# Performance work log

Hardware: AMD Instinct MI355X
Metric: run time of the kernel (lower is better)

## Reference

```python
import jax, jax.numpy as jnp
import numpy as np

N = 16384      # number of nodes (= in_num_dim)
F_DIM = 512    # node feature dim (= in_node_dim)
EMBED = 128    # embed_dim (D1)
OUT = 64       # out_dim (final latent)
E = 524288     # number of edges (avg degree 32)
GAT_SLOPE = 0.5    # GATConv negative_slope
LRELU_SLOPE = 0.01 # F.leaky_relu default on embed


def setup_inputs() -> dict:
    key = jax.random.key(0)
    ks = jax.random.split(key, 10)
    x = jax.random.normal(ks[0], (N, F_DIM), dtype=jnp.float32)
    edge_index = jax.random.randint(ks[1], (2, E), 0, N, dtype=jnp.int64)
    adj = jnp.zeros((1,), dtype=jnp.float32)  # unused by forward (as in source)
    # GATConv params (single head)
    W_gat = jax.random.normal(ks[2], (F_DIM, OUT), dtype=jnp.float32) / np.sqrt(F_DIM)
    att_src = jax.random.normal(ks[3], (OUT,), dtype=jnp.float32) * 0.1
    att_dst = jax.random.normal(ks[4], (OUT,), dtype=jnp.float32) * 0.1
    b_gat = jnp.zeros((OUT,), dtype=jnp.float32)
    # AttributeAE params: dense1 (N -> EMBED), dense2 (EMBED -> OUT)
    W1 = jax.random.normal(ks[5], (N, EMBED), dtype=jnp.float32) / np.sqrt(N)
    b1 = jnp.zeros((EMBED,), dtype=jnp.float32)
    W2 = jax.random.normal(ks[6], (EMBED, OUT), dtype=jnp.float32) / np.sqrt(EMBED)
    b2 = jnp.zeros((OUT,), dtype=jnp.float32)
    return dict(x=x, edge_index=edge_index, adj=adj, W_gat=W_gat,
                att_src=att_src, att_dst=att_dst, b_gat=b_gat,
                W1=W1, b1=b1, W2=W2, b2=b2)


def _gat_conv(x, edge_index, W_gat, att_src, att_dst, b_gat):
    # PyG GATConv, heads=1, with self-loops appended.
    n = x.shape[0]
    loops = jnp.arange(n, dtype=edge_index.dtype)
    src = jnp.concatenate([edge_index[0], loops])  # message sources j
    dst = jnp.concatenate([edge_index[1], loops])  # aggregation targets i
    h = x @ W_gat                                  # [N, OUT]
    a_src = h @ att_src                            # [N]
    a_dst = h @ att_dst                            # [N]
    e = jax.nn.leaky_relu(a_src[src] + a_dst[dst], GAT_SLOPE)  # [E+N]
    # segment softmax over incoming edges of each dst node
    m = jax.ops.segment_max(e, dst, num_segments=n)
    p = jnp.exp(e - m[dst])
    denom = jax.ops.segment_sum(p, dst, num_segments=n)
    alpha = p / denom[dst]
    out = jax.ops.segment_sum(alpha[:, None] * h[src], dst, num_segments=n)
    return out + b_gat


def _forward(x, edge_index, W_gat, att_src, att_dst, b_gat, W1, b1, W2, b2):
    # StructureAE
    embed_x = jax.nn.leaky_relu(
        _gat_conv(x, edge_index, W_gat, att_src, att_dst, b_gat), LRELU_SLOPE)
    A_hat = jax.nn.sigmoid(embed_x @ embed_x.T)          # [N, N]
    # AttributeAE (dropout = 0 -> identity)
    h1 = jax.nn.relu(x.T @ W1 + b1)                      # [F, EMBED]
    h2 = h1 @ W2 + b2                                    # [F, OUT]
    X_hat = embed_x @ h2.T                               # [N, F]
    return A_hat, X_hat


def reference(x, edge_index, adj, W_gat, att_src, att_dst, b_gat, W1, b1, W2, b2):
    # adj is accepted but unused, matching the torch forward signature
    return _forward(x, edge_index, W_gat, att_src, att_dst, b_gat, W1, b1, W2, b2)
```

## Files before the change

kernel.cpp:

```cpp
#include <hip/hip_runtime.h>
#include <hip/hip_bf16.h>

#define NN 16384
#define FD 512
#define EMB 128
#define OD 64
#define NE 524288

typedef __bf16 bf16x8 __attribute__((ext_vector_type(8)));
typedef float f32x4 __attribute__((ext_vector_type(4)));
typedef unsigned short u16;

__device__ inline float bfu2f(u16 u) {
    unsigned int x = (unsigned int)u << 16;
    float f;
    __builtin_memcpy(&f, &x, 4);
    return f;
}

__global__ __launch_bounds__(256) void k_prep(
    const float* __restrict__ x, __hip_bfloat16* __restrict__ xbf,
    const float* __restrict__ Wg, __hip_bfloat16* __restrict__ WgT,
    const int* __restrict__ ei, int* __restrict__ deg,
    const float* __restrict__ W1, float* __restrict__ part) {
    __shared__ float xs[4][64];
    __shared__ float wsh[4][EMB];
    int b = blockIdx.x;
    int t = threadIdx.x;
    if (b < 256) {
        int fb = b & 7, nc = b >> 3;
        int f0 = fb * 64, nb = nc * 512;
        int eb = (t & 15) * 8;
        int fbase = (t >> 4) * 4;
        float acc[4][8] = {};
        for (int n4 = 0; n4 < 512; n4 += 4) {
            { int nn = t >> 6, ff = t & 63;
              xs[nn][ff] = x[(size_t)(nb + n4 + nn) * FD + f0 + ff]; }
#pragma unroll
            for (int j = 0; j < 2; ++j) {
                int idx = t + j * 256;
                wsh[idx >> 7][idx & 127] = W1[(size_t)(nb + n4 + (idx >> 7)) * EMB + (idx & 127)];
            }
            __syncthreads();
#pragma unroll
            for (int nn = 0; nn < 4; ++nn) {
                float xv[4], wv[8];
#pragma unroll
                for (int i = 0; i < 4; ++i) xv[i] = xs[nn][fbase + i];
#pragma unroll
                for (int j = 0; j < 8; ++j) wv[j] = wsh[nn][eb + j];
#pragma unroll
                for (int i = 0; i < 4; ++i)
#pragma unroll
                    for (int j = 0; j < 8; ++j) acc[i][j] += xv[i] * wv[j];
            }
            __syncthreads();
        }
#pragma unroll
        for (int i = 0; i < 4; ++i) {
            float* dst = &part[((size_t)nc * FD + f0 + fbase + i) * EMB + eb];
            *reinterpret_cast<f32x4*>(dst) = *reinterpret_cast<f32x4*>(&acc[i][0]);
            *reinterpret_cast<f32x4*>(dst + 4) = *reinterpret_cast<f32x4*>(&acc[i][4]);
        }
        return;
    }
    b -= 256;
    if (b < NE / 256) {
        int i = b * 256 + t;
        atomicAdd(deg + ei[NE + i], 1);
        return;
    }
    b -= NE / 256;
    if (b < NN * FD / 2048) {
        size_t i = ((size_t)b * 256 + t) * 8;
        float4 v0 = *reinterpret_cast<const float4*>(x + i);
        float4 v1 = *reinterpret_cast<const float4*>(x + i + 4);
        __hip_bfloat16 o[8];
        o[0] = __float2bfloat16(v0.x); o[1] = __float2bfloat16(v0.y);
        o[2] = __float2bfloat16(v0.z); o[3] = __float2bfloat16(v0.w);
        o[4] = __float2bfloat16(v1.x); o[5] = __float2bfloat16(v1.y);
        o[6] = __float2bfloat16(v1.z); o[7] = __float2bfloat16(v1.w);
        *reinterpret_cast<uint4*>(xbf + i) = *reinterpret_cast<const uint4*>(o);
        return;
    }
    b -= NN * FD / 2048;
    {
        int c = t >> 2;
        int k0 = (t & 3) * 128;
        for (int j = 0; j < 128; ++j)
            WgT[c * 512 + k0 + j] = __float2bfloat16(Wg[(size_t)(k0 + j) * OD + c]);
    }
}

__global__ __launch_bounds__(256) void k_scan(const int* __restrict__ deg,
                                              int* __restrict__ row_start) {
    __shared__ int part[256];
    int t = threadIdx.x;
    int base = t * 64;
    int s = 0;
    for (int j = 0; j < 64; ++j) s += deg[base + j];
    part[t] = s;
    __syncthreads();
    for (int off = 1; off < 256; off <<= 1) {
        int v = (t >= off) ? part[t - off] : 0;
        __syncthreads();
        part[t] += v;
        __syncthreads();
    }
    int run = part[t] - s;
    if (t == 255) row_start[NN] = part[255];
    for (int j = 0; j < 64; ++j) { row_start[base + j] = run; run += deg[base + j]; }
}

__global__ __launch_bounds__(256) void k_mid(
    const int* __restrict__ ei, const int* __restrict__ row_start,
    int* __restrict__ cursor, int* __restrict__ ssrc,
    const __hip_bfloat16* __restrict__ xbf, const __hip_bfloat16* __restrict__ WgT,
    const float* __restrict__ att_s, const float* __restrict__ att_d,
    __hip_bfloat16* __restrict__ hbf, float* __restrict__ a_src, float* __restrict__ a_dst,
    const float* __restrict__ part, const float* __restrict__ b1,
    const float* __restrict__ W2, const float* __restrict__ b2,
    __hip_bfloat16* __restrict__ h2bf) {
    __shared__ float hv[4][EMB];
    int b = blockIdx.x;
    int t = threadIdx.x;
    if (b < NE / 256) {
        int i = b * 256 + t;
        int d = ei[NE + i];
        int pos = atomicAdd(cursor + d, 1);
        ssrc[row_start[d] + pos] = ei[i];
        return;
    }
    b -= NE / 256;
    int w = t >> 6, l = t & 63;
    if (b < NN / 64) {
        int lg = l >> 4, lm = l & 15;
        int r0 = b * 64 + w * 16;
        const bf16x8* Xp = reinterpret_cast<const bf16x8*>(xbf);
        const bf16x8* Wp = reinterpret_cast<const bf16x8*>(WgT);
        bf16x8 a[16];
        size_t abase = (size_t)(r0 + lm) * 64 + lg;
#pragma unroll
        for (int kc = 0; kc < 16; ++kc) a[kc] = Xp[abase + kc * 4];
        f32x4 acc[4];
#pragma unroll
        for (int j = 0; j < 4; ++j) {
            f32x4 c = {0.f, 0.f, 0.f, 0.f};
            size_t bbase = (size_t)(j * 16 + lm) * 64 + lg;
#pragma unroll
            for (int kc = 0; kc < 16; ++kc)
                c = __builtin_amdgcn_mfma_f32_16x16x32_bf16(a[kc], Wp[bbase + kc * 4], c, 0, 0, 0);
            acc[j] = c;
        }
#pragma unroll
        for (int j = 0; j < 4; ++j)
#pragma unroll
            for (int reg = 0; reg < 4; ++reg)
                hbf[(size_t)(r0 + lg * 4 + reg) * OD + j * 16 + lm] = __float2bfloat16(acc[j][reg]);
        float ats0 = att_s[lm], ats1 = att_s[16 + lm], ats2 = att_s[32 + lm], ats3 = att_s[48 + lm];
        float atd0 = att_d[lm], atd1 = att_d[16 + lm], atd2 = att_d[32 + lm], atd3 = att_d[48 + lm];
#pragma unroll
        for (int reg = 0; reg < 4; ++reg) {
            float ps = acc[0][reg] * ats0 + acc[1][reg] * ats1 + acc[2][reg] * ats2 + acc[3][reg] * ats3;
            float pd = acc[0][reg] * atd0 + acc[1][reg] * atd1 + acc[2][reg] * atd2 + acc[3][reg] * atd3;
#pragma unroll
            for (int off = 1; off < 16; off <<= 1) {
                ps += __shfl_xor(ps, off, 64);
                pd += __shfl_xor(pd, off, 64);
            }
            if (lm == 0) {
                int r = r0 + lg * 4 + reg;
                a_src[r] = ps;
                a_dst[r] = pd;
            }
        }
        return;
    }
    b -= NN / 64;
    {
        int f = b * 4 + w;
        float s0 = 0.f, s1 = 0.f;
        for (int nc = 0; nc < 32; ++nc) {
            const float* p = part + ((size_t)nc * FD + f) * EMB;
            s0 += p[l];
            s1 += p[l + 64];
        }
        s0 += b1[l]; s1 += b1[l + 64];
        hv[w][l] = s0 > 0.f ? s0 : 0.f;
        hv[w][l + 64] = s1 > 0.f ? s1 : 0.f;
        __syncthreads();
        float acc = b2[l];
        const float* myhv = hv[w];
        for (int e = 0; e < EMB; ++e)
            acc += myhv[e] * W2[e * OD + l];
        h2bf[(size_t)f * OD + l] = __float2bfloat16(acc);
    }
}

__global__ __launch_bounds__(256) void k_aggcsr(
    const int* __restrict__ row_start, const int* __restrict__ ssrc,
    const float* __restrict__ a_src, const float* __restrict__ a_dst,
    const u16* __restrict__ hb, const float* __restrict__ bg,
    __hip_bfloat16* __restrict__ ebf) {
    int node = blockIdx.x * 4 + (threadIdx.x >> 6);
    int lane = threadIdx.x & 63;
    float ad = a_dst[node];
    float e0 = a_src[node] + ad;
    e0 = e0 > 0.f ? e0 : 0.5f * e0;
    float p0 = __expf(e0);
    float denom = p0;
    float acc = p0 * bfu2f(hb[(size_t)node * OD + lane]);
    int j0 = row_start[node], j1 = row_start[node + 1];
    int j = j0;
    for (; j + 2 <= j1; j += 2) {
        int sA = ssrc[j], sB = ssrc[j + 1];
        float hA = bfu2f(hb[(size_t)sA * OD + lane]);
        float hB = bfu2f(hb[(size_t)sB * OD + lane]);
        float eA = a_src[sA] + ad, eB = a_src[sB] + ad;
        eA = eA > 0.f ? eA : 0.5f * eA;
        eB = eB > 0.f ? eB : 0.5f * eB;
        float pA = __expf(eA), pB = __expf(eB);
        denom += pA + pB;
        acc += pA * hA + pB * hB;
    }
    if (j < j1) {
        int s = ssrc[j];
        float e = a_src[s] + ad;
        e = e > 0.f ? e : 0.5f * e;
        float pv = __expf(e);
        denom += pv;
        acc += pv * bfu2f(hb[(size_t)s * OD + lane]);
    }
    float v = acc * __builtin_amdgcn_rcpf(denom) + bg[lane];
    v = v > 0.f ? v : 0.01f * v;
    ebf[(size_t)node * OD + lane] = __float2bfloat16(v);
}

__global__ __launch_bounds__(256) void k_mmX(const __hip_bfloat16* __restrict__ A,
                                             const __hip_bfloat16* __restrict__ B,
                                             float* __restrict__ out) {
    __shared__ float ls[4][32 * 68];
    int w = threadIdx.x >> 6, l = threadIdx.x & 63;
    int lg = l >> 4, lm = l & 15;
    int i0 = blockIdx.y * 128 + w * 32;
    int j0 = blockIdx.x * 128;
    const bf16x8* Ap = reinterpret_cast<const bf16x8*>(A);
    const bf16x8* Bp = reinterpret_cast<const bf16x8*>(B);
    size_t arow = (size_t)(i0 + lm) * 8;
    bf16x8 a0 = Ap[arow + lg];
    bf16x8 a1 = Ap[arow + 4 + lg];
    bf16x8 a2 = Ap[arow + 128 + lg];
    bf16x8 a3 = Ap[arow + 128 + 4 + lg];
    f32x4 accL[8], accH[8];
#pragma unroll
    for (int ct = 0; ct < 8; ++ct) {
        size_t brow = (size_t)(j0 + ct * 16 + lm) * 8;
        bf16x8 b0 = Bp[brow + lg];
        bf16x8 b1 = Bp[brow + 4 + lg];
        f32x4 cL = {0.f, 0.f, 0.f, 0.f};
        f32x4 cH = {0.f, 0.f, 0.f, 0.f};
        cL = __builtin_amdgcn_mfma_f32_16x16x32_bf16(a0, b0, cL, 0, 0, 0);
        cL = __builtin_amdgcn_mfma_f32_16x16x32_bf16(a1, b1, cL, 0, 0, 0);
        cH = __builtin_amdgcn_mfma_f32_16x16x32_bf16(a2, b0, cH, 0, 0, 0);
        cH = __builtin_amdgcn_mfma_f32_16x16x32_bf16(a3, b1, cH, 0, 0, 0);
        accL[ct] = cL;
        accH[ct] = cH;
    }
    float* myl = ls[w];
#pragma unroll
    for (int ph = 0; ph < 2; ++ph) {
        if (ph == 1) {
            asm volatile("s_waitcnt lgkmcnt(0)" ::: "memory");
            __builtin_amdgcn_sched_barrier(0);
        }
#pragma unroll
        for (int c4 = 0; c4 < 4; ++c4) {
            int ct = ph * 4 + c4;
            int col = c4 * 16 + lm;
#pragma unroll
            for (int reg = 0; reg < 4; ++reg) {
                int row = lg * 4 + reg;
                myl[row * 68 + col] = accL[ct][reg];
                myl[(row + 16) * 68 + col] = accH[ct][reg];
            }
        }
        asm volatile("s_waitcnt lgkmcnt(0)" ::: "memory");
        __builtin_amdgcn_sched_barrier(0);
#pragma unroll
        for (int i = 0; i < 8; ++i) {
            int row = i * 4 + lg;
            f32x4 v = *reinterpret_cast<const f32x4*>(&myl[row * 68 + lm * 4]);
            float* dst = &out[(size_t)(i0 + row) * FD + j0 + ph * 64 + lm * 4];
            __builtin_nontemporal_store(v, reinterpret_cast<f32x4*>(dst));
        }
    }
}

__global__ __launch_bounds__(256) void k_mmA(const __hip_bfloat16* __restrict__ A,
                                             float* __restrict__ out) {
    __shared__ float ls[4][32 * 68];
    int bid = blockIdx.x;
    int swz = (bid & 7) * 2048 + (bid >> 3);
    int rowT = swz >> 7;
    int colT = swz & 127;
    int w = threadIdx.x >> 6, l = threadIdx.x & 63;
    int lg = l >> 4, lm = l & 15;
    int i0 = rowT * 128 + w * 32;
    int j0 = colT * 128;
    const bf16x8* Ap = reinterpret_cast<const bf16x8*>(A);
    size_t arow = (size_t)(i0 + lm) * 8;
    bf16x8 a0 = Ap[arow + lg];
    bf16x8 a1 = Ap[arow + 4 + lg];
    bf16x8 a2 = Ap[arow + 128 + lg];
    bf16x8 a3 = Ap[arow + 128 + 4 + lg];
    f32x4 accL[8], accH[8];
#pragma unroll
    for (int ct = 0; ct < 8; ++ct) {
        size_t brow = (size_t)(j0 + ct * 16 + lm) * 8;
        bf16x8 b0 = Ap[brow + lg];
        bf16x8 b1 = Ap[brow + 4 + lg];
        f32x4 cL = {0.f, 0.f, 0.f, 0.f};
        f32x4 cH = {0.f, 0.f, 0.f, 0.f};
        cL = __builtin_amdgcn_mfma_f32_16x16x32_bf16(a0, b0, cL, 0, 0, 0);
        cL = __builtin_amdgcn_mfma_f32_16x16x32_bf16(a1, b1, cL, 0, 0, 0);
        cH = __builtin_amdgcn_mfma_f32_16x16x32_bf16(a2, b0, cH, 0, 0, 0);
        cH = __builtin_amdgcn_mfma_f32_16x16x32_bf16(a3, b1, cH, 0, 0, 0);
        accL[ct] = cL;
        accH[ct] = cH;
    }
    float* myl = ls[w];
#pragma unroll
    for (int ph = 0; ph < 2; ++ph) {
        if (ph == 1) {
            asm volatile("s_waitcnt lgkmcnt(0)" ::: "memory");
            __builtin_amdgcn_sched_barrier(0);
        }
#pragma unroll
        for (int c4 = 0; c4 < 4; ++c4) {
            int ct = ph * 4 + c4;
            int col = c4 * 16 + lm;
#pragma unroll
            for (int reg = 0; reg < 4; ++reg) {
                float vL = accL[ct][reg], vH = accH[ct][reg];
                vL = __builtin_amdgcn_rcpf(1.f + __expf(-vL));
                vH = __builtin_amdgcn_rcpf(1.f + __expf(-vH));
                int row = lg * 4 + reg;
                myl[row * 68 + col] = vL;
                myl[(row + 16) * 68 + col] = vH;
            }
        }
        asm volatile("s_waitcnt lgkmcnt(0)" ::: "memory");
        __builtin_amdgcn_sched_barrier(0);
#pragma unroll
        for (int i = 0; i < 8; ++i) {
            int row = i * 4 + lg;
            f32x4 v = *reinterpret_cast<const f32x4*>(&myl[row * 68 + lm * 4]);
            float* dst = &out[(size_t)(i0 + row) * NN + j0 + ph * 64 + lm * 4];
            __builtin_nontemporal_store(v, reinterpret_cast<f32x4*>(dst));
        }
    }
}

extern "C" void kernel_launch(void* const* d_in, const int* in_sizes, int n_in,
                              void* d_out, int out_size, void* d_ws, size_t ws_size,
                              hipStream_t stream) {
    const float* x     = (const float*)d_in[0];
    const int*   ei    = (const int*)d_in[1];
    const float* Wg    = (const float*)d_in[3];
    const float* att_s = (const float*)d_in[4];
    const float* att_d = (const float*)d_in[5];
    const float* bg    = (const float*)d_in[6];
    const float* W1    = (const float*)d_in[7];
    const float* b1    = (const float*)d_in[8];
    const float* W2    = (const float*)d_in[9];
    const float* b2    = (const float*)d_in[10];

    float* ws    = (float*)d_ws;
    float* a_src = ws;
    float* a_dst = a_src + NN;
    int*   deg   = (int*)(a_dst + NN);
    int*   cursor= deg + NN;
    int*   row_start = cursor + NN;
    int*   ssrc  = row_start + NN + 4;
    float* part  = (float*)(ssrc + NE);
    __hip_bfloat16* xbf  = (__hip_bfloat16*)(part + 32 * FD * EMB);
    __hip_bfloat16* WgT  = xbf + (size_t)NN * FD;
    __hip_bfloat16* hbf  = WgT + (size_t)OD * FD;
    __hip_bfloat16* ebf  = hbf + (size_t)NN * OD;
    __hip_bfloat16* h2bf = ebf + (size_t)NN * OD;

    float* Ahat = (float*)d_out;
    float* Xhat = Ahat + (size_t)NN * NN;

    hipMemsetAsync(deg, 0, 2 * NN * sizeof(int), stream);
    const int prep_blocks = 256 + NE / 256 + NN * FD / 2048 + 1;
    k_prep<<<prep_blocks, 256, 0, stream>>>(x, xbf, Wg, WgT, ei, deg, W1, part);
    k_scan<<<1, 256, 0, stream>>>(deg, row_start);
    const int mid_blocks = NE / 256 + NN / 64 + FD / 4;
    k_mid<<<mid_blocks, 256, 0, stream>>>(ei, row_start, cursor, ssrc,
                                          xbf, WgT, att_s, att_d,
                                          hbf, a_src, a_dst,
                                          part, b1, W2, b2, h2bf);
    k_aggcsr<<<NN / 4, 256, 0, stream>>>(row_start, ssrc, a_src, a_dst,
                                         (const u16*)hbf, bg, ebf);
    k_mmX<<<dim3(FD / 128, NN / 128), 256, 0, stream>>>(ebf, h2bf, Xhat);
    k_mmA<<<NN / 128 * (NN / 128), 256, 0, stream>>>(ebf, Ahat);
}
```

Baseline: 424.6 us.

## Merge X_hat and A_hat matmuls into one launch with wider-row stores

Combines the X_hat and A_hat GEMM kernels into a single launch, where the first 512 blocks compute X_hat and the rest compute A_hat. This removes one kernel launch and the gap between the two. The A_hat epilogue now stages 16 rows × 128 columns per phase, so each wave writes full 512-byte row segments instead of 256-byte halves. The block-index swizzle for A_hat is dropped in favour of plain row-major tile order, which may change L2 reuse of the ebf rows.

```diff
diff --git a/kernel.cpp b/kernel.cpp
--- a/kernel.cpp
+++ b/kernel.cpp
@@ -236,78 +236,72 @@
     ebf[(size_t)node * OD + lane] = __float2bfloat16(v);
 }
 
-__global__ __launch_bounds__(256) void k_mmX(const __hip_bfloat16* __restrict__ A,
-                                             const __hip_bfloat16* __restrict__ B,
-                                             float* __restrict__ out) {
-    __shared__ float ls[4][32 * 68];
+__global__ __launch_bounds__(256) void k_mmAX(const __hip_bfloat16* __restrict__ ebf,
+                                              const __hip_bfloat16* __restrict__ h2bf,
+                                              float* __restrict__ outA,
+                                              float* __restrict__ outX) {
+    __shared__ float ls[4][2176];
     int w = threadIdx.x >> 6, l = threadIdx.x & 63;
     int lg = l >> 4, lm = l & 15;
-    int i0 = blockIdx.y * 128 + w * 32;
-    int j0 = blockIdx.x * 128;
-    const bf16x8* Ap = reinterpret_cast<const bf16x8*>(A);
-    const bf16x8* Bp = reinterpret_cast<const bf16x8*>(B);
-    size_t arow = (size_t)(i0 + lm) * 8;
-    bf16x8 a0 = Ap[arow + lg];
-    bf16x8 a1 = Ap[arow + 4 + lg];
-    bf16x8 a2 = Ap[arow + 128 + lg];
-    bf16x8 a3 = Ap[arow + 128 + 4 + lg];
-    f32x4 accL[8], accH[8];
-#pragma unroll
-    for (int ct = 0; ct < 8; ++ct) {
-        size_t brow = (size_t)(j0 + ct * 16 + lm) * 8;
-        bf16x8 b0 = Bp[brow + lg];
-        bf16x8 b1 = Bp[brow + 4 + lg];
-        f32x4 cL = {0.f, 0.f, 0.f, 0.f};
-        f32x4 cH = {0.f, 0.f, 0.f, 0.f};
-        cL = __builtin_amdgcn_mfma_f32_16x16x32_bf16(a0, b0, cL, 0, 0, 0);
-        cL = __builtin_amdgcn_mfma_f32_16x16x32_bf16(a1, b1, cL, 0, 0, 0);
-        cH = __builtin_amdgcn_mfma_f32_16x16x32_bf16(a2, b0, cH, 0, 0, 0);
-        cH = __builtin_amdgcn_mfma_f32_16x16x32_bf16(a3, b1, cH, 0, 0, 0);
-        accL[ct] = cL;
-        accH[ct] = cH;
-    }
     float* myl = ls[w];
-#pragma unroll
-    for (int ph = 0; ph < 2; ++ph) {
-        if (ph == 1) {
+    const bf16x8* Ap = reinterpret_cast<const bf16x8*>(ebf);
+    if (blockIdx.x < 512) {
+        int bid = blockIdx.x;
+        int i0 = (bid >> 2) * 128 + w * 32;
+        int j0 = (bid & 3) * 128;
+        const bf16x8* Bp = reinterpret_cast<const bf16x8*>(h2bf);
+        size_t arow = (size_t)(i0 + lm) * 8;
+        bf16x8 a0 = Ap[arow + lg];
+        bf16x8 a1 = Ap[arow + 4 + lg];
+        bf16x8 a2 = Ap[arow + 128 + lg];
+        bf16x8 a3 = Ap[arow + 128 + 4 + lg];
+        f32x4 accL[8], accH[8];
+#pragma unroll
+        for (int ct = 0; ct < 8; ++ct) {
+            size_t brow = (size_t)(j0 + ct * 16 + lm) * 8;
+            bf16x8 b0 = Bp[brow + lg];
+            bf16x8 b1 = Bp[brow + 4 + lg];
+            f32x4 cL = {0.f, 0.f, 0.f, 0.f};
+            f32x4 cH = {0.f, 0.f, 0.f, 0.f};
+            cL = __builtin_amdgcn_mfma_f32_16x16x32_bf16(a0, b0, cL, 0, 0, 0);
+            cL = __builtin_amdgcn_mfma_f32_16x16x32_bf16(a1, b1, cL, 0, 0, 0);
+            cH = __builtin_amdgcn_mfma_f32_16x16x32_bf16(a2, b0, cH, 0, 0, 0);
+            cH = __builtin_amdgcn_mfma_f32_16x16x32_bf16(a3, b1, cH, 0, 0, 0);
+            accL[ct] = cL;
+            accH[ct] = cH;
+        }
+#pragma unroll
+        for (int ph = 0; ph < 2; ++ph) {
+            if (ph == 1) {
+                asm volatile("s_waitcnt lgkmcnt(0)" ::: "memory");
+                __builtin_amdgcn_sched_barrier(0);
+            }
+#pragma unroll
+            for (int c4 = 0; c4 < 4; ++c4) {
+                int ct = ph * 4 + c4;
+                int col = c4 * 16 + lm;
+#pragma unroll
+                for (int reg = 0; reg < 4; ++reg) {
+                    int row = lg * 4 + reg;
+                    myl[row * 68 + col] = accL[ct][reg];
+                    myl[(row + 16) * 68 + col] = accH[ct][reg];
+                }
+            }
             asm volatile("s_waitcnt lgkmcnt(0)" ::: "memory");
             __builtin_amdgcn_sched_barrier(0);
-        }
-#pragma unroll
-        for (int c4 = 0; c4 < 4; ++c4) {
-            int ct = ph * 4 + c4;
-            int col = c4 * 16 + lm;
-#pragma unroll
-            for (int reg = 0; reg < 4; ++reg) {
-                int row = lg * 4 + reg;
-                myl[row * 68 + col] = accL[ct][reg];
-                myl[(row + 16) * 68 + col] = accH[ct][reg];
-            }
-        }
-        asm volatile("s_waitcnt lgkmcnt(0)" ::: "memory");
-        __builtin_amdgcn_sched_barrier(0);
-#pragma unroll
-        for (int i = 0; i < 8; ++i) {
-            int row = i * 4 + lg;
-            f32x4 v = *reinterpret_cast<const f32x4*>(&myl[row * 68 + lm * 4]);
-            float* dst = &out[(size_t)(i0 + row) * FD + j0 + ph * 64 + lm * 4];
-            __builtin_nontemporal_store(v, reinterpret_cast<f32x4*>(dst));
-        }
-    }
-}
-
-__global__ __launch_bounds__(256) void k_mmA(const __hip_bfloat16* __restrict__ A,
-                                             float* __restrict__ out) {
-    __shared__ float ls[4][32 * 68];
-    int bid = blockIdx.x;
-    int swz = (bid & 7) * 2048 + (bid >> 3);
-    int rowT = swz >> 7;
-    int colT = swz & 127;
-    int w = threadIdx.x >> 6, l = threadIdx.x & 63;
-    int lg = l >> 4, lm = l & 15;
-    int i0 = rowT * 128 + w * 32;
-    int j0 = colT * 128;
-    const bf16x8* Ap = reinterpret_cast<const bf16x8*>(A);
+#pragma unroll
+            for (int i = 0; i < 8; ++i) {
+                int row = i * 4 + lg;
+                f32x4 v = *reinterpret_cast<const f32x4*>(&myl[row * 68 + lm * 4]);
+                float* dst = &outX[(size_t)(i0 + row) * FD + j0 + ph * 64 + lm * 4];
+                __builtin_nontemporal_store(v, reinterpret_cast<f32x4*>(dst));
+            }
+        }
+        return;
+    }
+    int bid = blockIdx.x - 512;
+    int i0 = (bid >> 7) * 128 + w * 32;
+    int j0 = (bid & 127) * 128;
     size_t arow = (size_t)(i0 + lm) * 8;
     bf16x8 a0 = Ap[arow + lg];
     bf16x8 a1 = Ap[arow + 4 + lg];
@@ -328,7 +322,6 @@
         accL[ct] = cL;
         accH[ct] = cH;
     }
-    float* myl = ls[w];
 #pragma unroll
     for (int ph = 0; ph < 2; ++ph) {
         if (ph == 1) {
@@ -336,26 +329,23 @@
             __builtin_amdgcn_sched_barrier(0);
         }
 #pragma unroll
-        for (int c4 = 0; c4 < 4; ++c4) {
-            int ct = ph * 4 + c4;
-            int col = c4 * 16 + lm;
+        for (int ct = 0; ct < 8; ++ct) {
+            int col = ct * 16 + lm;
 #pragma unroll
             for (int reg = 0; reg < 4; ++reg) {
-                float vL = accL[ct][reg], vH = accH[ct][reg];
-                vL = __builtin_amdgcn_rcpf(1.f + __expf(-vL));
-                vH = __builtin_amdgcn_rcpf(1.f + __expf(-vH));
-                int row = lg * 4 + reg;
-                myl[row * 68 + col] = vL;
-                myl[(row + 16) * 68 + col] = vH;
+                float v = ph ? accH[ct][reg] : accL[ct][reg];
+                v = __builtin_amdgcn_rcpf(1.f + __expf(-v));
+                myl[(lg * 4 + reg) * 132 + col] = v;
             }
         }
         asm volatile("s_waitcnt lgkmcnt(0)" ::: "memory");
         __builtin_amdgcn_sched_barrier(0);
 #pragma unroll
         for (int i = 0; i < 8; ++i) {
-            int row = i * 4 + lg;
-            f32x4 v = *reinterpret_cast<const f32x4*>(&myl[row * 68 + lm * 4]);
-            float* dst = &out[(size_t)(i0 + row) * NN + j0 + ph * 64 + lm * 4];
+            int row = i * 2 + (l >> 5);
+            int c4 = (l & 31) * 4;
+            f32x4 v = *reinterpret_cast<const f32x4*>(&myl[row * 132 + c4]);
+            float* dst = &outA[(size_t)(i0 + ph * 16 + row) * NN + j0 + c4];
             __builtin_nontemporal_store(v, reinterpret_cast<f32x4*>(dst));
         }
     }
@@ -403,6 +393,5 @@
                                           part, b1, W2, b2, h2bf);
     k_aggcsr<<<NN / 4, 256, 0, stream>>>(row_start, ssrc, a_src, a_dst,
                                          (const u16*)hbf, bg, ebf);
-    k_mmX<<<dim3(FD / 128, NN / 128), 256, 0, stream>>>(ebf, h2bf, Xhat);
-    k_mmA<<<NN / 128 * (NN / 128), 256, 0, stream>>>(ebf, Ahat);
-}
+    k_mmAX<<<512 + (NN / 128) * (NN / 128), 256, 0, stream>>>(ebf, h2bf, Ahat, Xhat);
+}
```

Result: faster. 405.5 us (-4.5%).
